# Performance work log

Hardware: AMD Instinct MI355X
Metric: run time of the kernel (lower is better)

Reference implementation:

```python
import jax, jax.numpy as jnp
import numpy as np

MAX_LEN = 2048
D_MODEL = 1024
NUM_HEADS = 16
D_HEAD = D_MODEL // NUM_HEADS
BATCH = 2
SEQ = 2048


def setup_inputs() -> dict:
    key = jax.random.key(0)
    ks = jax.random.split(key, 8)
    scale = 1.0 / np.sqrt(D_MODEL)
    return {
        "x": jax.random.normal(ks[0], (BATCH, SEQ, D_MODEL), dtype=jnp.float32),
        "Wq": jax.random.normal(ks[1], (D_MODEL, D_MODEL), dtype=jnp.float32) * scale,
        "bq": jnp.zeros((D_MODEL,), dtype=jnp.float32),
        "Wk": jax.random.normal(ks[2], (D_MODEL, D_MODEL), dtype=jnp.float32) * scale,
        "bk": jnp.zeros((D_MODEL,), dtype=jnp.float32),
        "Wv": jax.random.normal(ks[3], (D_MODEL, D_MODEL), dtype=jnp.float32) * scale,
        "bv": jnp.zeros((D_MODEL,), dtype=jnp.float32),
        "Er": jax.random.normal(ks[4], (MAX_LEN, D_HEAD), dtype=jnp.float32),
    }


def _skew(QEr):
    # QEr: [B, H, S, S] -> Transformer-XL skew -> Srel: [B, H, S, S]
    B, H, S, _ = QEr.shape
    padded = jnp.pad(QEr, ((0, 0), (0, 0), (0, 0), (1, 0)))  # [B,H,S,S+1]
    reshaped = padded.reshape(B, H, S + 1, S)
    return reshaped[:, :, 1:, :]


def reference(x, Wq, bq, Wk, bk, Wv, bv, Er):
    B, S, D = x.shape
    H, dh = NUM_HEADS, D // NUM_HEADS
    q = (x @ Wq + bq).reshape(B, S, H, dh).transpose(0, 2, 1, 3)  # [B,H,S,dh]
    k = (x @ Wk + bk).reshape(B, S, H, dh).transpose(0, 2, 1, 3)
    v = (x @ Wv + bv).reshape(B, S, H, dh).transpose(0, 2, 1, 3)
    Er_s = Er[MAX_LEN - S:, :]                                    # [S, dh]
    QEr = jnp.einsum("bhsd,ld->bhsl", q, Er_s)                    # [B,H,S,S]
    Srel = _skew(QEr)
    QKt = jnp.einsum("bhsd,bhtd->bhst", q, k)
    attn = (QKt + Srel) / jnp.sqrt(jnp.asarray(dh, x.dtype))
    causal = jnp.tril(jnp.ones((S, S), dtype=bool))
    attn = jnp.where(causal[None, None], attn, -jnp.inf)
    attn = jax.nn.softmax(attn, axis=-1)
    out = jnp.einsum("bhst,bhtd->bhsd", attn, v)                  # [B,H,S,dh]
    return out.transpose(0, 2, 1, 3).reshape(B, S, D)             # dropout in eval = identity
```

## Files before the change

kernel.cpp:

```cpp
#include <hip/hip_runtime.h>
#include <hip/hip_bf16.h>

#define SLEN   2048
#define DMODEL 1024
#define NHEADS 16
#define DHEAD  64
#define NBATCH 2
#define EPAD_ROWS 2432

typedef __bf16 bf16x8 __attribute__((ext_vector_type(8)));
typedef float  f32x4  __attribute__((ext_vector_type(4)));

__device__ __forceinline__ unsigned short f2bf(float f) {
    unsigned int u = __builtin_bit_cast(unsigned int, f);
    return (unsigned short)((u + 0x7fffu + ((u >> 16) & 1u)) >> 16);
}

__device__ __forceinline__ unsigned short f2bf_hw(float f) {
    return __builtin_bit_cast(unsigned short, (__bf16)f);
}

__device__ __forceinline__ bf16x8 ld8(const unsigned short* p) {
    union { uint4 u; bf16x8 b; } t;
    t.u = *(const uint4*)p;
    return t.b;
}

__device__ __forceinline__ void glds16(const unsigned short* g, unsigned short* l) {
    __builtin_amdgcn_global_load_lds(
        (const __attribute__((address_space(1))) unsigned int*)g,
        (__attribute__((address_space(3))) unsigned int*)l, 16, 0, 0);
}

__global__ __launch_bounds__(256) void prep_kernel(
    const float* __restrict__ x, const float* __restrict__ Er,
    const float* __restrict__ Wq, const float* __restrict__ Wk,
    const float* __restrict__ Wv,
    unsigned short* __restrict__ xb, unsigned short* __restrict__ Ep,
    unsigned short* __restrict__ Wt) {
    const int bi = blockIdx.x, tid = threadIdx.x;
    if (bi < 4096) {
        int i = (bi * 256 + tid) * 4;
        float4 v = *(const float4*)(x + i);
        ushort4 o;
        o.x = f2bf(v.x); o.y = f2bf(v.y); o.z = f2bf(v.z); o.w = f2bf(v.w);
        *(ushort4*)(xb + i) = o;
    } else if (bi < 4704) {
        int i = (bi - 4096) * 256 + tid;
        int row = i >> 6;
        unsigned short v = 0;
        if (row < SLEN) v = f2bf(Er[i]);
        Ep[i] = v;
    } else {
        __shared__ float tile[32][33];
        const int b3 = bi - 4704;
        const int z = b3 >> 10, rem = b3 & 1023;
        const int n0 = (rem & 31) * 32, k0 = (rem >> 5) * 32;
        const float* W = (z == 0) ? Wq : (z == 1 ? Wk : Wv);
        unsigned short* out = Wt + (size_t)z * DMODEL * DMODEL;
        const int tx = tid & 31, ty = tid >> 5;
        for (int r = 0; r < 32; r += 8)
            tile[ty + r][tx] = W[(size_t)(k0 + ty + r) * DMODEL + n0 + tx];
        __syncthreads();
        for (int r = 0; r < 32; r += 8)
            out[(size_t)(n0 + ty + r) * DMODEL + k0 + tx] = f2bf(tile[tx][ty + r]);
    }
}

__global__ __launch_bounds__(256) void qkv_gemm(
    const unsigned short* __restrict__ xb, const unsigned short* __restrict__ Wt,
    const float* __restrict__ bq, const float* __restrict__ bk, const float* __restrict__ bv,
    unsigned short* __restrict__ Qs, unsigned short* __restrict__ Ks,
    unsigned short* __restrict__ Vts) {
    const int z = blockIdx.z;
    const float* bias = (z == 0) ? bq : (z == 1 ? bk : bv);
    const unsigned short* Wz = Wt + (size_t)z * DMODEL * DMODEL;
    const int m0 = blockIdx.y * 128, n0 = blockIdx.x * 128;

    __shared__ __align__(16) unsigned short As[2][128][64];
    __shared__ __align__(16) unsigned short Bs[2][128][64];

    const int tid = threadIdx.x;
    const int wave = tid >> 6, lane = tid & 63, l16 = lane & 15, quad = lane >> 4;
    const int wm = (wave >> 1) * 64, wn = (wave & 1) * 64;

    const int lr8 = lane >> 3;
    const int sc  = ((lane & 7) ^ lr8) * 8;

    f32x4 acc[4][4];
#pragma unroll
    for (int mi = 0; mi < 4; mi++)
#pragma unroll
        for (int ni = 0; ni < 4; ni++) acc[mi][ni] = (f32x4){0.f, 0.f, 0.f, 0.f};

#pragma unroll
    for (int c = 0; c < 4; c++) {
        const int seg = wave * 4 + c;
        const int r8  = seg * 8 + lr8;
        glds16(&xb[(size_t)(m0 + r8) * DMODEL + sc], &As[0][seg * 8][0]);
        glds16(&Wz[(size_t)(n0 + r8) * DMODEL + sc], &Bs[0][seg * 8][0]);
    }
    __syncthreads();

    for (int j = 0; j < 16; ++j) {
        const int cur = j & 1;
        if (j < 15) {
            const int k1 = (j + 1) * 64, nb = cur ^ 1;
#pragma unroll
            for (int c = 0; c < 4; c++) {
                const int seg = wave * 4 + c;
                const int r8  = seg * 8 + lr8;
                glds16(&xb[(size_t)(m0 + r8) * DMODEL + k1 + sc], &As[nb][seg * 8][0]);
                glds16(&Wz[(size_t)(n0 + r8) * DMODEL + k1 + sc], &Bs[nb][seg * 8][0]);
            }
        }
        const unsigned short (*Aarr)[64] = (z == 2) ? Bs[cur] : As[cur];
        const unsigned short (*Barr)[64] = (z == 2) ? As[cur] : Bs[cur];
#pragma unroll
        for (int ks = 0; ks < 2; ks++) {
            const int pc = ((ks * 4 + quad) ^ (l16 & 7)) * 8;
            bf16x8 a[4], b[4];
#pragma unroll
            for (int mi = 0; mi < 4; mi++) a[mi] = ld8(&Aarr[wm + mi * 16 + l16][pc]);
#pragma unroll
            for (int ni = 0; ni < 4; ni++) b[ni] = ld8(&Barr[wn + ni * 16 + l16][pc]);
#pragma unroll
            for (int mi = 0; mi < 4; mi++)
#pragma unroll
                for (int ni = 0; ni < 4; ni++)
                    acc[mi][ni] = __builtin_amdgcn_mfma_f32_16x16x32_bf16(a[mi], b[ni], acc[mi][ni], 0, 0, 0);
        }
        __syncthreads();
    }

    if (z == 2) {
#pragma unroll
        for (int mi = 0; mi < 4; mi++)
#pragma unroll
            for (int r = 0; r < 4; r++) {
                const int n = n0 + wm + mi * 16 + quad * 4 + r;
                const float bb = bias[n];
                const int h = n >> 6, d = n & 63;
#pragma unroll
                for (int ni = 0; ni < 4; ni++) {
                    const int m = m0 + wn + ni * 16 + l16;
                    const int bi = m >> 11, s = m & 2047;
                    Vts[((size_t)((bi * NHEADS + h) * 64 + d)) * SLEN + s] = f2bf(acc[mi][ni][r] + bb);
                }
            }
    } else {
#pragma unroll
        for (int ni = 0; ni < 4; ni++) {
            const int n = n0 + wn + ni * 16 + l16;
            const float bb = bias[n];
            const int h = n >> 6, d = n & 63;
#pragma unroll
            for (int mi = 0; mi < 4; mi++)
#pragma unroll
                for (int r = 0; r < 4; r++) {
                    const int m = m0 + wm + mi * 16 + quad * 4 + r;
                    const int bi = m >> 11, s = m & 2047;
                    float v = acc[mi][ni][r] + bb;
                    if (z == 0)
                        Qs[((size_t)(bi * NHEADS + h) * SLEN + s) * 64 + d] = f2bf(v * 0.125f);
                    else
                        Ks[((size_t)(bi * NHEADS + h) * SLEN + s) * 64 + d] = f2bf(v);
                }
        }
    }
}

__global__ __launch_bounds__(256, 2) void attn_kernel(
    const unsigned short* __restrict__ Q,
    const unsigned short* __restrict__ K,
    const unsigned short* __restrict__ Vt,
    const unsigned short* __restrict__ Ep,
    float* __restrict__ out) {
    const int tid = threadIdx.x;
    const int wave = tid >> 6, lane = tid & 63, l16 = lane & 15, quad = lane >> 4;
    const int lr8 = lane >> 3;
    const int swz = ((lane & 7) ^ lr8) * 8;

    const int bh = blockIdx.x & 31;
    const int pg = blockIdx.x >> 5;

    __shared__ __align__(16) unsigned short Ksh[2][64 * 64];
    __shared__ __align__(16) unsigned short Vsh[2][64 * 64];
    __shared__ __align__(16) unsigned short Esh[256 * 64];
    __shared__ __align__(16) unsigned short Pg[4][16][88];

    const unsigned short* Qb = Q + (size_t)bh * SLEN * 64;
    const unsigned short* Kb = K + (size_t)bh * SLEN * 64;
    const unsigned short* Vb = Vt + (size_t)bh * 64 * SLEN;
    const int ob = bh >> 4, oh = bh & 15;

    const int pc0 = (quad ^ (l16 & 7)) * 8;
    const int pc1 = ((4 + quad) ^ (l16 & 7)) * 8;
    int perm[4];
    bool hi[4];
#pragma unroll
    for (int r = 0; r < 4; r++) {
        const int row16 = quad * 4 + r;
        perm[r] = (quad << 4) | ((l16 + 15 - row16) & 15);
        hi[r] = (l16 + row16 >= 15);
    }

    int s0 = pg * 64;
    int ntp = pg + 1;

#pragma unroll 1
    for (int pass = 0; pass < 2; ++pass) {
        const int sw = s0 + 16 * wave;
        const bf16x8 aq0 = ld8(Qb + (size_t)(sw + l16) * 64 + quad * 8);
        const bf16x8 aq1 = ld8(Qb + (size_t)(sw + l16) * 64 + 32 + quad * 8);

        f32x4 accO[4];
        float sacc[4];
#pragma unroll
        for (int nt = 0; nt < 4; nt++) accO[nt] = (f32x4){0.f, 0.f, 0.f, 0.f};
#pragma unroll
        for (int r = 0; r < 4; r++) sacc[r] = 0.f;

        const int p0row = SLEN - 64 - s0;

#pragma unroll
        for (int c = 0; c < 2; c++) {
            const int seg = wave * 2 + c;
            glds16(&Kb[(size_t)(seg * 8 + lr8) * 64 + swz], &Ksh[0][seg * 8 * 64]);
            glds16(&Vb[(size_t)(seg * 8 + lr8) * SLEN + swz], &Vsh[0][seg * 8 * 64]);
        }
#pragma unroll
        for (int u = 0; u < 6; u++) {
            const int idx = wave * 6 + u;
            const int grow = p0row + idx * 8;
            glds16(&Ep[(size_t)(grow + lr8) * 64 + swz], &Esh[(grow & 255) * 64]);
        }
        __syncthreads();

        for (int j = 0; j < ntp; ++j) {
            const int t0 = j * 64;
            const int cur = j & 1;

            if (j + 1 < ntp) {
                const int t1 = t0 + 64, nb = cur ^ 1;
#pragma unroll
                for (int c = 0; c < 2; c++) {
                    const int seg = wave * 2 + c;
                    glds16(&Kb[(size_t)(t1 + seg * 8 + lr8) * 64 + swz], &Ksh[nb][seg * 8 * 64]);
                    glds16(&Vb[(size_t)(seg * 8 + lr8) * SLEN + t1 + swz], &Vsh[nb][seg * 8 * 64]);
                }
                const int er = p0row + t0 + 128;
#pragma unroll
                for (int c = 0; c < 2; c++) {
                    const int seg = wave * 2 + c;
                    glds16(&Ep[(size_t)(er + seg * 8 + lr8) * 64 + swz],
                           &Esh[((er + seg * 8) & 255) * 64]);
                }
            }

            f32x4 accS[4];
#pragma unroll
            for (int nt = 0; nt < 4; nt++) accS[nt] = (f32x4){0.f, 0.f, 0.f, 0.f};
#pragma unroll
            for (int nt = 0; nt < 4; nt++) {
                bf16x8 bk0 = ld8(&Ksh[cur][(nt * 16 + l16) * 64 + pc0]);
                bf16x8 bk1 = ld8(&Ksh[cur][(nt * 16 + l16) * 64 + pc1]);
                accS[nt] = __builtin_amdgcn_mfma_f32_16x16x32_bf16(aq0, bk0, accS[nt], 0, 0, 0);
                accS[nt] = __builtin_amdgcn_mfma_f32_16x16x32_bf16(aq1, bk1, accS[nt], 0, 0, 0);
            }

            const int rm0 = (SLEN - 16 - sw + t0) & 255;
            f32x4 accE[5];
#pragma unroll
            for (int nt = 0; nt < 5; nt++) accE[nt] = (f32x4){0.f, 0.f, 0.f, 0.f};
#pragma unroll
            for (int nt = 0; nt < 5; nt++) {
                const int rowm = (rm0 + nt * 16 + l16) & 255;
                bf16x8 be0 = ld8(&Esh[rowm * 64 + pc0]);
                bf16x8 be1 = ld8(&Esh[rowm * 64 + pc1]);
                accE[nt] = __builtin_amdgcn_mfma_f32_16x16x32_bf16(aq0, be0, accE[nt], 0, 0, 0);
                accE[nt] = __builtin_amdgcn_mfma_f32_16x16x32_bf16(aq1, be1, accE[nt], 0, 0, 0);
            }

            auto scoreblk = [&](bool masked) {
#pragma unroll
                for (int nt = 0; nt < 4; nt++) {
#pragma unroll
                    for (int r = 0; r < 4; r++) {
                        float send = hi[r] ? accE[nt][r] : accE[nt + 1][r];
                        float rel = __shfl(send, perm[r]);
                        float pexp = __expf(accS[nt][r] + rel - 16.0f);
                        if (masked)
                            pexp = (t0 + nt * 16 + l16 <= sw + quad * 4 + r) ? pexp : 0.0f;
                        sacc[r] += pexp;
                        Pg[wave][quad * 4 + r][nt * 16 + l16] = f2bf_hw(pexp);
                    }
                }
            };
            if (t0 + 63 <= sw) scoreblk(false);
            else               scoreblk(true);

            bf16x8 a0 = ld8(&Pg[wave][l16][quad * 8]);
            bf16x8 a1 = ld8(&Pg[wave][l16][32 + quad * 8]);
#pragma unroll
            for (int nt = 0; nt < 4; nt++) {
                bf16x8 bv0 = ld8(&Vsh[cur][(nt * 16 + l16) * 64 + pc0]);
                bf16x8 bv1 = ld8(&Vsh[cur][(nt * 16 + l16) * 64 + pc1]);
                accO[nt] = __builtin_amdgcn_mfma_f32_16x16x32_bf16(a0, bv0, accO[nt], 0, 0, 0);
                accO[nt] = __builtin_amdgcn_mfma_f32_16x16x32_bf16(a1, bv1, accO[nt], 0, 0, 0);
            }

            __syncthreads();
        }

#pragma unroll
        for (int r = 0; r < 4; r++) {
            float s4 = sacc[r];
#pragma unroll
            for (int off = 1; off < 16; off <<= 1) s4 += __shfl_xor(s4, off);
            const float inv = 1.f / s4;
            const int s = sw + quad * 4 + r;
#pragma unroll
            for (int nt = 0; nt < 4; nt++)
                out[((size_t)(ob * SLEN + s)) * DMODEL + oh * 64 + nt * 16 + l16] =
                    accO[nt][r] * inv;
        }

        s0 = (31 - pg) * 64;
        ntp = 32 - pg;
    }
}

extern "C" void kernel_launch(void* const* d_in, const int* in_sizes, int n_in,
                              void* d_out, int out_size, void* d_ws, size_t ws_size,
                              hipStream_t stream) {
    const float* x  = (const float*)d_in[0];
    const float* Wq = (const float*)d_in[1];
    const float* bq = (const float*)d_in[2];
    const float* Wk = (const float*)d_in[3];
    const float* bk = (const float*)d_in[4];
    const float* Wv = (const float*)d_in[5];
    const float* bv = (const float*)d_in[6];
    const float* Er = (const float*)d_in[7];
    float* out = (float*)d_out;

    char* p = (char*)d_ws;
    unsigned short* xb  = (unsigned short*)p; p += (size_t)4096 * 1024 * 2;
    unsigned short* Wt  = (unsigned short*)p; p += (size_t)3 * 1024 * 1024 * 2;
    unsigned short* Qs  = (unsigned short*)p; p += (size_t)32 * 2048 * 64 * 2;
    unsigned short* Ks  = (unsigned short*)p; p += (size_t)32 * 2048 * 64 * 2;
    unsigned short* Vts = (unsigned short*)p; p += (size_t)32 * 2048 * 64 * 2;
    unsigned short* Ep  = (unsigned short*)p; p += (size_t)EPAD_ROWS * 64 * 2;

    hipLaunchKernelGGL(prep_kernel, dim3(7776), dim3(256), 0, stream,
                       x, Er, Wq, Wk, Wv, xb, Ep, Wt);
    hipLaunchKernelGGL(qkv_gemm, dim3(8, 32, 3), dim3(256), 0, stream,
                       xb, Wt, bq, bk, bv, Qs, Ks, Vts);
    hipLaunchKernelGGL(attn_kernel, dim3(512), dim3(256), 0, stream, Qs, Ks, Vts, Ep, out);
}
```

Before: 188.5 us.

## Fuse Q/K/V projections into one GEMM kernel sharing the x tile

Replaces the three-way z-dimension QKV GEMM launch with a single kernel in which each block loads an x tile once and multiplies it against the Wq, Wk and Wv tiles, keeping three accumulator sets. This cuts redundant global loads and LDS fills of x and reduces the block count from 768 to 256. In exchange, register pressure triples (192 accumulator floats per lane), LDS use doubles to 128KB, occupancy drops to one block per CU, and fewer blocks than before are available to fill the machine. Output rounding also switches to the hardware bf16 conversion.

```diff
diff --git a/kernel.cpp b/kernel.cpp
--- a/kernel.cpp
+++ b/kernel.cpp
@@ -67,38 +67,47 @@
     }
 }
 
-__global__ __launch_bounds__(256) void qkv_gemm(
+__global__ __launch_bounds__(256, 1) void qkv_fused(
     const unsigned short* __restrict__ xb, const unsigned short* __restrict__ Wt,
     const float* __restrict__ bq, const float* __restrict__ bk, const float* __restrict__ bv,
     unsigned short* __restrict__ Qs, unsigned short* __restrict__ Ks,
     unsigned short* __restrict__ Vts) {
-    const int z = blockIdx.z;
-    const float* bias = (z == 0) ? bq : (z == 1 ? bk : bv);
-    const unsigned short* Wz = Wt + (size_t)z * DMODEL * DMODEL;
     const int m0 = blockIdx.y * 128, n0 = blockIdx.x * 128;
-
-    __shared__ __align__(16) unsigned short As[2][128][64];
-    __shared__ __align__(16) unsigned short Bs[2][128][64];
+    const unsigned short* Wqp = Wt;
+    const unsigned short* Wkp = Wt + (size_t)DMODEL * DMODEL;
+    const unsigned short* Wvp = Wt + (size_t)2 * DMODEL * DMODEL;
+
+    __shared__ __align__(16) unsigned short As [2][128][64];
+    __shared__ __align__(16) unsigned short Bqs[2][128][64];
+    __shared__ __align__(16) unsigned short Bks[2][128][64];
+    __shared__ __align__(16) unsigned short Bvs[2][128][64];
 
     const int tid = threadIdx.x;
     const int wave = tid >> 6, lane = tid & 63, l16 = lane & 15, quad = lane >> 4;
     const int wm = (wave >> 1) * 64, wn = (wave & 1) * 64;
-
     const int lr8 = lane >> 3;
     const int sc  = ((lane & 7) ^ lr8) * 8;
-
-    f32x4 acc[4][4];
+    const int pc0 = (quad ^ (l16 & 7)) * 8;
+    const int pc1 = ((4 + quad) ^ (l16 & 7)) * 8;
+
+    f32x4 accQ[4][4], accK[4][4], accV[4][4];
 #pragma unroll
     for (int mi = 0; mi < 4; mi++)
 #pragma unroll
-        for (int ni = 0; ni < 4; ni++) acc[mi][ni] = (f32x4){0.f, 0.f, 0.f, 0.f};
+        for (int ni = 0; ni < 4; ni++) {
+            accQ[mi][ni] = (f32x4){0.f, 0.f, 0.f, 0.f};
+            accK[mi][ni] = (f32x4){0.f, 0.f, 0.f, 0.f};
+            accV[mi][ni] = (f32x4){0.f, 0.f, 0.f, 0.f};
+        }
 
 #pragma unroll
     for (int c = 0; c < 4; c++) {
         const int seg = wave * 4 + c;
         const int r8  = seg * 8 + lr8;
-        glds16(&xb[(size_t)(m0 + r8) * DMODEL + sc], &As[0][seg * 8][0]);
-        glds16(&Wz[(size_t)(n0 + r8) * DMODEL + sc], &Bs[0][seg * 8][0]);
+        glds16(&xb [(size_t)(m0 + r8) * DMODEL + sc], &As [0][seg * 8][0]);
+        glds16(&Wqp[(size_t)(n0 + r8) * DMODEL + sc], &Bqs[0][seg * 8][0]);
+        glds16(&Wkp[(size_t)(n0 + r8) * DMODEL + sc], &Bks[0][seg * 8][0]);
+        glds16(&Wvp[(size_t)(n0 + r8) * DMODEL + sc], &Bvs[0][seg * 8][0]);
     }
     __syncthreads();
 
@@ -110,64 +119,75 @@
             for (int c = 0; c < 4; c++) {
                 const int seg = wave * 4 + c;
                 const int r8  = seg * 8 + lr8;
-                glds16(&xb[(size_t)(m0 + r8) * DMODEL + k1 + sc], &As[nb][seg * 8][0]);
-                glds16(&Wz[(size_t)(n0 + r8) * DMODEL + k1 + sc], &Bs[nb][seg * 8][0]);
-            }
-        }
-        const unsigned short (*Aarr)[64] = (z == 2) ? Bs[cur] : As[cur];
-        const unsigned short (*Barr)[64] = (z == 2) ? As[cur] : Bs[cur];
+                glds16(&xb [(size_t)(m0 + r8) * DMODEL + k1 + sc], &As [nb][seg * 8][0]);
+                glds16(&Wqp[(size_t)(n0 + r8) * DMODEL + k1 + sc], &Bqs[nb][seg * 8][0]);
+                glds16(&Wkp[(size_t)(n0 + r8) * DMODEL + k1 + sc], &Bks[nb][seg * 8][0]);
+                glds16(&Wvp[(size_t)(n0 + r8) * DMODEL + k1 + sc], &Bvs[nb][seg * 8][0]);
+            }
+        }
 #pragma unroll
         for (int ks = 0; ks < 2; ks++) {
-            const int pc = ((ks * 4 + quad) ^ (l16 & 7)) * 8;
-            bf16x8 a[4], b[4];
-#pragma unroll
-            for (int mi = 0; mi < 4; mi++) a[mi] = ld8(&Aarr[wm + mi * 16 + l16][pc]);
-#pragma unroll
-            for (int ni = 0; ni < 4; ni++) b[ni] = ld8(&Barr[wn + ni * 16 + l16][pc]);
+            const int pc = ks ? pc1 : pc0;
+            bf16x8 xa[4], b[4];
+#pragma unroll
+            for (int mi = 0; mi < 4; mi++) xa[mi] = ld8(&As[cur][wm + mi * 16 + l16][pc]);
+#pragma unroll
+            for (int ni = 0; ni < 4; ni++) b[ni] = ld8(&Bqs[cur][wn + ni * 16 + l16][pc]);
 #pragma unroll
             for (int mi = 0; mi < 4; mi++)
 #pragma unroll
                 for (int ni = 0; ni < 4; ni++)
-                    acc[mi][ni] = __builtin_amdgcn_mfma_f32_16x16x32_bf16(a[mi], b[ni], acc[mi][ni], 0, 0, 0);
+                    accQ[mi][ni] = __builtin_amdgcn_mfma_f32_16x16x32_bf16(xa[mi], b[ni], accQ[mi][ni], 0, 0, 0);
+#pragma unroll
+            for (int ni = 0; ni < 4; ni++) b[ni] = ld8(&Bks[cur][wn + ni * 16 + l16][pc]);
+#pragma unroll
+            for (int mi = 0; mi < 4; mi++)
+#pragma unroll
+                for (int ni = 0; ni < 4; ni++)
+                    accK[mi][ni] = __builtin_amdgcn_mfma_f32_16x16x32_bf16(xa[mi], b[ni], accK[mi][ni], 0, 0, 0);
+#pragma unroll
+            for (int ni = 0; ni < 4; ni++) b[ni] = ld8(&Bvs[cur][wn + ni * 16 + l16][pc]);
+#pragma unroll
+            for (int mi = 0; mi < 4; mi++)
+#pragma unroll
+                for (int ni = 0; ni < 4; ni++)
+                    accV[ni][mi] = __builtin_amdgcn_mfma_f32_16x16x32_bf16(b[ni], xa[mi], accV[ni][mi], 0, 0, 0);
         }
         __syncthreads();
     }
 
-    if (z == 2) {
+#pragma unroll
+    for (int ni = 0; ni < 4; ni++) {
+        const int n = n0 + wn + ni * 16 + l16;
+        const float bbq = bq[n], bbk = bk[n];
+        const int h = n >> 6, d = n & 63;
 #pragma unroll
         for (int mi = 0; mi < 4; mi++)
 #pragma unroll
             for (int r = 0; r < 4; r++) {
-                const int n = n0 + wm + mi * 16 + quad * 4 + r;
-                const float bb = bias[n];
-                const int h = n >> 6, d = n & 63;
-#pragma unroll
-                for (int ni = 0; ni < 4; ni++) {
-                    const int m = m0 + wn + ni * 16 + l16;
-                    const int bi = m >> 11, s = m & 2047;
-                    Vts[((size_t)((bi * NHEADS + h) * 64 + d)) * SLEN + s] = f2bf(acc[mi][ni][r] + bb);
-                }
-            }
-    } else {
-#pragma unroll
-        for (int ni = 0; ni < 4; ni++) {
-            const int n = n0 + wn + ni * 16 + l16;
-            const float bb = bias[n];
+                const int m = m0 + wm + mi * 16 + quad * 4 + r;
+                const int bi = m >> 11, s = m & 2047;
+                Qs[((size_t)(bi * NHEADS + h) * SLEN + s) * 64 + d] =
+                    f2bf_hw((accQ[mi][ni][r] + bbq) * 0.125f);
+                Ks[((size_t)(bi * NHEADS + h) * SLEN + s) * 64 + d] =
+                    f2bf_hw(accK[mi][ni][r] + bbk);
+            }
+    }
+#pragma unroll
+    for (int ni = 0; ni < 4; ni++)
+#pragma unroll
+        for (int r = 0; r < 4; r++) {
+            const int n = n0 + wn + ni * 16 + quad * 4 + r;
+            const float bbv = bv[n];
             const int h = n >> 6, d = n & 63;
 #pragma unroll
-            for (int mi = 0; mi < 4; mi++)
-#pragma unroll
-                for (int r = 0; r < 4; r++) {
-                    const int m = m0 + wm + mi * 16 + quad * 4 + r;
-                    const int bi = m >> 11, s = m & 2047;
-                    float v = acc[mi][ni][r] + bb;
-                    if (z == 0)
-                        Qs[((size_t)(bi * NHEADS + h) * SLEN + s) * 64 + d] = f2bf(v * 0.125f);
-                    else
-                        Ks[((size_t)(bi * NHEADS + h) * SLEN + s) * 64 + d] = f2bf(v);
-                }
-        }
-    }
+            for (int mi = 0; mi < 4; mi++) {
+                const int m = m0 + wm + mi * 16 + l16;
+                const int bi = m >> 11, s = m & 2047;
+                Vts[((size_t)((bi * NHEADS + h) * 64 + d)) * SLEN + s] =
+                    f2bf_hw(accV[ni][mi][r] + bbv);
+            }
+        }
 }
 
 __global__ __launch_bounds__(256, 2) void attn_kernel(
@@ -354,7 +374,7 @@
 
     hipLaunchKernelGGL(prep_kernel, dim3(7776), dim3(256), 0, stream,
                        x, Er, Wq, Wk, Wv, xb, Ep, Wt);
-    hipLaunchKernelGGL(qkv_gemm, dim3(8, 32, 3), dim3(256), 0, stream,
+    hipLaunchKernelGGL(qkv_fused, dim3(8, 32), dim3(256), 0, stream,
                        xb, Wt, bq, bk, bv, Qs, Ks, Vts);
     hipLaunchKernelGGL(attn_kernel, dim3(512), dim3(256), 0, stream, Qs, Ks, Vts, Ep, out);
 }
```

Result: no change. 189.4 us (+0.5%).
